# Performance work log

Measured on AMD Instinct MI355X. Metric: run time of the kernel, lower is better.

The kernel has to match this reference:

```python
import jax, jax.numpy as jnp
import numpy as np

LR = 0.1          # RMSprop learning rate (set_hyper_parameters)
ALPHA = 0.9       # RMSprop decay
ITERATIONS = 5    # SVGD iterations
INV_SIG2 = 1.0    # Gaussian posterior score scale (concrete post_grad)
EPS = 1e-8


def setup_inputs() -> dict:
    key = jax.random.key(0)
    k1, k2 = jax.random.split(key)
    x = jax.random.normal(k1, (8, 2048, 8), dtype=jnp.float32)          # [B, N, D] particles
    observation = jax.random.normal(k2, (8, 8), dtype=jnp.float32)      # [B, D]
    return {"x": x, "observation": observation}


def _svgd(x, observation):
    B, N, D = x.shape
    # median heuristic bandwidth h = median(pairwise dist)^2 / log(N), per batch, no-grad
    sq = jnp.sum((x[:, :, None, :] - x[:, None, :, :]) ** 2, axis=-1)   # [B, N, N]
    med = jnp.median(jnp.sqrt(sq).reshape(B, -1), axis=-1)              # [B]
    h = jax.lax.stop_gradient(med ** 2 / jnp.log(jnp.float32(N)))       # [B]
    inv_N = jnp.float32(1.0 / N)

    def post_grad(xc):
        # Gaussian posterior score: d/dx log N(x; observation, sigma^2 I)
        return (observation[:, None, :] - xc) * INV_SIG2                # [B, N, D]

    def step(carry, _):
        xc, s = carry
        dist = xc[:, :, None, :] - xc[:, None, :, :]                    # [B, i, j, D]
        K = jnp.exp(-jnp.sum(dist ** 2, axis=-1) / h[:, None, None])    # [B, i, j] rbf
        g = post_grad(xc)                                               # [B, j, D]
        # phi_i = (1/N) sum_j [ K_ij * g_j + (2/h)(x_i - x_j) K_ij ]
        phi = inv_N * (jnp.einsum('bij,bjd->bid', K, g)
                       + (2.0 / h)[:, None, None] * jnp.einsum('bij,bijd->bid', K, dist))
        # RMSprop (state update under no_grad in the original)
        s = jax.lax.stop_gradient(ALPHA * s + (1.0 - ALPHA) * phi ** 2)
        xc = xc + LR * phi / (jnp.sqrt(s) + EPS)
        return (xc, s), None

    (x, _), _ = jax.lax.scan(step, (x, jnp.zeros_like(x)), None, length=ITERATIONS)
    return x


def reference(x, observation):
    return _svgd(x, observation)
```

## Files before the change

### kernel.cpp

```cpp
#include <hip/hip_runtime.h>
#include <cstdint>

#define BATCH 8
#define NPART 2048
#define DDIM 8
#define NN (NPART * NPART)

#define MJCHUNK 128
#define SJCHUNK 512

constexpr float LR = 0.1f;
constexpr float ALPHA = 0.9f;
constexpr float EPS = 1e-8f;
constexpr float INV_N = 1.0f / (float)NPART;
constexpr float LOG2E = 1.44269504088896340736f;

typedef float v2f __attribute__((ext_vector_type(2)));
typedef float v4f __attribute__((ext_vector_type(4)));

__global__ __launch_bounds__(256) void init_ws_k(unsigned* __restrict__ hist,
                                                 unsigned* __restrict__ prefix,
                                                 unsigned* __restrict__ rank) {
    const int tid = blockIdx.x * 256 + threadIdx.x;
    if (tid < BATCH * 2 * 256) hist[tid] = 0u;
    if (tid < BATCH * 2) {
        prefix[tid] = 0u;
        rank[tid] = (unsigned)(NN / 2) + (unsigned)(tid & 1);
    }
}

__global__ __launch_bounds__(256) void median_hist_k(const float* __restrict__ x,
                                                     unsigned* __restrict__ hist,
                                                     const unsigned* __restrict__ prefix,
                                                     int shift) {
    __shared__ __align__(16) v4f xs0[MJCHUNK];
    __shared__ __align__(16) v4f xs1[MJCHUNK];
    __shared__ float rs[MJCHUNK];
    __shared__ unsigned lh[256 * 32];

    const int b = blockIdx.x;
    const int tid = threadIdx.x;
    const int lane = tid & 63;
    const int slot = tid & 31;
    const int trow = tid >> 6;
    const float* xb = x + (size_t)b * NPART * DDIM;

    const unsigned p0 = prefix[2 * b + 0];
    const unsigned p1 = prefix[2 * b + 1];
    const bool same = (p0 == p1);
    const unsigned mask = (shift == 24) ? 0u : (0xFFFFFFFFu << (shift + 8));

    const int nsel = same ? 1 : 2;
    for (int sel = 0; sel < nsel; ++sel) {
        const unsigned pref = sel ? p1 : p0;
        __syncthreads();
        for (int t = tid; t < 256 * 32; t += 256) lh[t] = 0u;

        for (int sp = 0; sp < 2; ++sp) {
            const int strip = sp ? (255 - (int)blockIdx.y) : (int)blockIdx.y;
            const int ibase = strip * 8 + trow * 2;
            v2f xi[2][4];
            float q[2];
#pragma unroll
            for (int rr = 0; rr < 2; ++rr) {
                const v4f t0 = ((const v4f*)(xb + (size_t)(ibase + rr) * DDIM))[0];
                const v4f t1 = ((const v4f*)(xb + (size_t)(ibase + rr) * DDIM))[1];
                xi[rr][0] = t0.xy; xi[rr][1] = t0.zw;
                xi[rr][2] = t1.xy; xi[rr][3] = t1.zw;
                q[rr] = t0.x * t0.x + t0.y * t0.y + t0.z * t0.z + t0.w * t0.w
                      + t1.x * t1.x + t1.y * t1.y + t1.z * t1.z + t1.w * t1.w;
            }
            const int c0 = (strip >> 4) * MJCHUNK;
            for (int cbase = c0; cbase < NPART; cbase += MJCHUNK) {
                __syncthreads();
                for (int t = tid; t < MJCHUNK; t += 256) {
                    const v4f u0 = ((const v4f*)(xb + (size_t)(cbase + t) * DDIM))[0];
                    const v4f u1 = ((const v4f*)(xb + (size_t)(cbase + t) * DDIM))[1];
                    xs0[t] = u0;
                    xs1[t] = u1;
                    rs[t] = u0.x * u0.x + u0.y * u0.y + u0.z * u0.z + u0.w * u0.w
                          + u1.x * u1.x + u1.y * u1.y + u1.z * u1.z + u1.w * u1.w;
                }
                __syncthreads();
#pragma unroll
                for (int j = lane; j < MJCHUNK; j += 64) {
                    const int jg = cbase + j;
                    const v4f A = xs0[j];
                    const v4f B = xs1[j];
                    const float r = rs[j];
                    const v2f A0 = A.xy, A1 = A.zw, B0 = B.xy, B1 = B.zw;
#pragma unroll
                    for (int rr = 0; rr < 2; ++rr) {
                        v2f p = A0 * xi[rr][0];
                        p += A1 * xi[rr][1];
                        p += B0 * xi[rr][2];
                        p += B1 * xi[rr][3];
                        const float sq = fmaxf(fmaf(-2.0f, p.x + p.y, q[rr] + r), 0.0f);
                        const unsigned u = __float_as_uint(sq);
                        if (jg > ibase + rr && (u & mask) == pref)
                            atomicAdd(&lh[((u >> shift) & 255u) * 32 + slot], 2u);
                    }
                }
            }
        }
        __syncthreads();
        unsigned tot = 0;
#pragma unroll
        for (int sct = 0; sct < 32; ++sct) tot += lh[tid * 32 + ((sct + tid) & 31)];
        if (tot) {
            atomicAdd(&hist[b * 512 + sel * 256 + tid], tot);
            if (same) atomicAdd(&hist[b * 512 + 256 + tid], tot);
        }
    }
}

__global__ void median_scan_k(unsigned* __restrict__ hist,
                              unsigned* __restrict__ prefix,
                              unsigned* __restrict__ rank,
                              int shift,
                              float* __restrict__ hpar) {
    __shared__ unsigned selv[16];
    const int t = threadIdx.x;
    if (t < 16) {
        const unsigned r = rank[t];
        const unsigned pref = prefix[t];
        const unsigned* hb = hist + t * 256;
        unsigned cum = 0;
        int bin = 0;
        for (; bin < 256; ++bin) {
            unsigned c = hb[bin];
            if (bin == 0 && pref == 0u) c += (unsigned)NPART;
            if (cum + c >= r) break;
            cum += c;
        }
        if (bin > 255) bin = 255;
        const unsigned np = pref | ((unsigned)bin << shift);
        prefix[t] = np;
        rank[t] = r - cum;
        selv[t] = np;
    }
    __syncthreads();
    for (int q = t; q < 16 * 256; q += 64) hist[q] = 0u;
    if (shift == 8 && t < BATCH) {
        const float v1 = __uint_as_float(selv[2 * t + 0]);
        const float v2 = __uint_as_float(selv[2 * t + 1]);
        const float med = 0.5f * (sqrtf(v1) + sqrtf(v2));
        const float h = (med * med) / logf((float)NPART);
        hpar[2 * t + 0] = -LOG2E / h;
        hpar[2 * t + 1] = 2.0f / h;
    }
}

__global__ __launch_bounds__(256, 4) void svgd_step_k(const float* __restrict__ x_in,
                                                      float* __restrict__ x_out,
                                                      float* __restrict__ s,
                                                      const float* __restrict__ hpar,
                                                      const float* __restrict__ obs,
                                                      int first) {
    __shared__ __align__(16) float smem[4608];
    v4f* xs0 = (v4f*)smem;
    v4f* xs1 = (v4f*)(smem + 2048);
    float* rs = smem + 4096;
    float (*part)[8][9] = (float (*)[8][9])smem;

    const int b = blockIdx.x;
    const int tid = threadIdx.x;
    const int lane = tid & 63;
    const int trow = tid >> 6;
    const float* xb = x_in + (size_t)b * NPART * DDIM;

    const float nih2 = hpar[2 * b + 0];
    const float c2 = hpar[2 * b + 1];
    const float cdot2 = -2.0f * nih2;

    const int ibase = blockIdx.y * 16 + trow * 4;
    v2f xi[4][4];
    float q[4];
#pragma unroll
    for (int rr = 0; rr < 4; ++rr) {
        const v4f t0 = ((const v4f*)(xb + (size_t)(ibase + rr) * DDIM))[0];
        const v4f t1 = ((const v4f*)(xb + (size_t)(ibase + rr) * DDIM))[1];
        xi[rr][0] = t0.xy; xi[rr][1] = t0.zw;
        xi[rr][2] = t1.xy; xi[rr][3] = t1.zw;
        q[rr] = nih2 * (t0.x * t0.x + t0.y * t0.y + t0.z * t0.z + t0.w * t0.w
                      + t1.x * t1.x + t1.y * t1.y + t1.z * t1.z + t1.w * t1.w);
    }

    float S0[4] = {0, 0, 0, 0};
    v2f V[4][4];
#pragma unroll
    for (int rr = 0; rr < 4; ++rr)
#pragma unroll
        for (int k = 0; k < 4; ++k) V[rr][k] = (v2f){0, 0};

    for (int cbase = 0; cbase < NPART; cbase += SJCHUNK) {
        __syncthreads();
        for (int t = tid; t < SJCHUNK; t += 256) {
            const v4f u0 = ((const v4f*)(xb + (size_t)(cbase + t) * DDIM))[0];
            const v4f u1 = ((const v4f*)(xb + (size_t)(cbase + t) * DDIM))[1];
            xs0[t] = u0;
            xs1[t] = u1;
            rs[t] = nih2 * (u0.x * u0.x + u0.y * u0.y + u0.z * u0.z + u0.w * u0.w
                          + u1.x * u1.x + u1.y * u1.y + u1.z * u1.z + u1.w * u1.w);
        }
        __syncthreads();
#pragma unroll 2
        for (int j = lane; j < SJCHUNK; j += 64) {
            const v4f A = xs0[j];
            const v4f B = xs1[j];
            const float r = rs[j];
            const v2f A0 = A.xy, A1 = A.zw, B0 = B.xy, B1 = B.zw;
#pragma unroll
            for (int rr = 0; rr < 4; ++rr) {
                v2f p = A0 * xi[rr][0];
                p += A1 * xi[rr][1];
                p += B0 * xi[rr][2];
                p += B1 * xi[rr][3];
                const float K = __builtin_amdgcn_exp2f(fmaf(cdot2, p.x + p.y, q[rr] + r));
                S0[rr] += K;
                const v2f K2 = {K, K};
                V[rr][0] += A0 * K2;
                V[rr][1] += A1 * K2;
                V[rr][2] += B0 * K2;
                V[rr][3] += B1 * K2;
            }
        }
    }

    __syncthreads();
#pragma unroll
    for (int rr = 0; rr < 4; ++rr) {
        float t0 = S0[rr];
        float t1 = V[rr][0].x, t2 = V[rr][0].y;
        float t3 = V[rr][1].x, t4 = V[rr][1].y;
        float t5 = V[rr][2].x, t6 = V[rr][2].y;
        float t7 = V[rr][3].x, t8 = V[rr][3].y;
        t0 += __shfl_xor(t0, 32); t0 += __shfl_xor(t0, 16); t0 += __shfl_xor(t0, 8);
        t1 += __shfl_xor(t1, 32); t1 += __shfl_xor(t1, 16); t1 += __shfl_xor(t1, 8);
        t2 += __shfl_xor(t2, 32); t2 += __shfl_xor(t2, 16); t2 += __shfl_xor(t2, 8);
        t3 += __shfl_xor(t3, 32); t3 += __shfl_xor(t3, 16); t3 += __shfl_xor(t3, 8);
        t4 += __shfl_xor(t4, 32); t4 += __shfl_xor(t4, 16); t4 += __shfl_xor(t4, 8);
        t5 += __shfl_xor(t5, 32); t5 += __shfl_xor(t5, 16); t5 += __shfl_xor(t5, 8);
        t6 += __shfl_xor(t6, 32); t6 += __shfl_xor(t6, 16); t6 += __shfl_xor(t6, 8);
        t7 += __shfl_xor(t7, 32); t7 += __shfl_xor(t7, 16); t7 += __shfl_xor(t7, 8);
        t8 += __shfl_xor(t8, 32); t8 += __shfl_xor(t8, 16); t8 += __shfl_xor(t8, 8);
        if (lane < 8) {
            const int row = trow * 4 + rr;
            part[row][lane][0] = t0;
            part[row][lane][1] = t1;
            part[row][lane][2] = t2;
            part[row][lane][3] = t3;
            part[row][lane][4] = t4;
            part[row][lane][5] = t5;
            part[row][lane][6] = t6;
            part[row][lane][7] = t7;
            part[row][lane][8] = t8;
        }
    }
    __syncthreads();

    if (tid < 128) {
        const int d2i = tid & 7;
        const int r2 = tid >> 3;
        const int i2 = blockIdx.y * 16 + r2;
        float S0t = 0.0f, Vt = 0.0f;
#pragma unroll
        for (int l = 0; l < 8; ++l) {
            S0t += part[r2][l][0];
            Vt += part[r2][l][1 + d2i];
        }
        const size_t idx = ((size_t)b * NPART + i2) * DDIM + d2i;
        const float xid = x_in[idx];
        const float obsd = obs[b * DDIM + d2i];
        const float U = fmaf(S0t, xid, -Vt);
        const float T = fmaf(S0t, obsd - xid, U);
        const float phi = INV_N * fmaf(c2, U, T);
        float sv;
        if (first) {
            sv = (1.0f - ALPHA) * phi * phi;
        } else {
            sv = ALPHA * s[idx] + (1.0f - ALPHA) * phi * phi;
        }
        s[idx] = sv;
        x_out[idx] = xid + LR * phi / (sqrtf(sv) + EPS);
    }
}

extern "C" void kernel_launch(void* const* d_in, const int* in_sizes, int n_in,
                              void* d_out, int out_size, void* d_ws, size_t ws_size,
                              hipStream_t stream) {
    const float* x0 = (const float*)d_in[0];
    const float* obs = (const float*)d_in[1];
    float* out = (float*)d_out;

    float* xa = (float*)d_ws;
    float* s = xa + BATCH * NPART * DDIM;
    unsigned* hist = (unsigned*)(s + BATCH * NPART * DDIM);
    unsigned* prefix = hist + BATCH * 2 * 256;
    unsigned* rank = prefix + BATCH * 2;
    float* hpar = (float*)(rank + BATCH * 2);

    init_ws_k<<<16, 256, 0, stream>>>(hist, prefix, rank);

    for (int r = 0; r < 3; ++r) {
        const int shift = 24 - 8 * r;
        median_hist_k<<<dim3(BATCH, 128), 256, 0, stream>>>(x0, hist, prefix, shift);
        median_scan_k<<<1, 64, 0, stream>>>(hist, prefix, rank, shift, hpar);
    }

    svgd_step_k<<<dim3(BATCH, 128), 256, 0, stream>>>(x0, out, s, hpar, obs, 1);
    svgd_step_k<<<dim3(BATCH, 128), 256, 0, stream>>>(out, xa, s, hpar, obs, 0);
    svgd_step_k<<<dim3(BATCH, 128), 256, 0, stream>>>(xa, out, s, hpar, obs, 0);
    svgd_step_k<<<dim3(BATCH, 128), 256, 0, stream>>>(out, xa, s, hpar, obs, 0);
    svgd_step_k<<<dim3(BATCH, 128), 256, 0, stream>>>(xa, out, s, hpar, obs, 0);
}
```

Baseline: 217.3 us.

## Compute pairwise RBF exponents with split-bf16 MFMA instead of scalar dot products

The SVGD step kernel now builds the exponent argument q_i + q_j - 2 x_i·x_j as a 32x32 matrix product on MFMA units. It splits each fp32 operand into bf16 high and low parts and uses three MFMAs to approximate fp32 accuracy. The norms are folded in through augmented columns. Each block now covers 32 rows with 512 threads, and each wave takes a 256-wide j range. The kernel reads x_j directly from global memory/L1 instead of staging it in LDS. This aims to offload the dot-product FLOPs from the VALU, at the risk of precision loss in the exponent and more uncoalesced global loads.

```diff
diff --git a/kernel.cpp b/kernel.cpp
--- a/kernel.cpp
+++ b/kernel.cpp
@@ -7,7 +7,6 @@
 #define NN (NPART * NPART)
 
 #define MJCHUNK 128
-#define SJCHUNK 512
 
 constexpr float LR = 0.1f;
 constexpr float ALPHA = 0.9f;
@@ -17,6 +16,17 @@
 
 typedef float v2f __attribute__((ext_vector_type(2)));
 typedef float v4f __attribute__((ext_vector_type(4)));
+typedef __attribute__((ext_vector_type(8))) short bf16x8;
+typedef __attribute__((ext_vector_type(16))) float f32x16;
+
+union FragU { bf16x8 v; unsigned u[4]; };
+
+__device__ __forceinline__ unsigned pk_bf16(float f0, float f1) {
+    return (__float_as_uint(f0) >> 16) | (__float_as_uint(f1) & 0xFFFF0000u);
+}
+__device__ __forceinline__ float btrunc(float f) {
+    return __uint_as_float(__float_as_uint(f) & 0xFFFF0000u);
+}
 
 __global__ __launch_bounds__(256) void init_ws_k(unsigned* __restrict__ hist,
                                                  unsigned* __restrict__ prefix,
@@ -151,123 +161,127 @@
     }
 }
 
-__global__ __launch_bounds__(256, 4) void svgd_step_k(const float* __restrict__ x_in,
+__global__ __launch_bounds__(512, 4) void svgd_step_k(const float* __restrict__ x_in,
                                                       float* __restrict__ x_out,
                                                       float* __restrict__ s,
                                                       const float* __restrict__ hpar,
                                                       const float* __restrict__ obs,
                                                       int first) {
-    __shared__ __align__(16) float smem[4608];
-    v4f* xs0 = (v4f*)smem;
-    v4f* xs1 = (v4f*)(smem + 2048);
-    float* rs = smem + 4096;
-    float (*part)[8][9] = (float (*)[8][9])smem;
+    __shared__ float part[32][16][9];
 
     const int b = blockIdx.x;
     const int tid = threadIdx.x;
-    const int lane = tid & 63;
-    const int trow = tid >> 6;
+    const int w = tid >> 6;
+    const int l = tid & 63;
+    const int col = l & 31;
+    const int half = l >> 5;
     const float* xb = x_in + (size_t)b * NPART * DDIM;
 
     const float nih2 = hpar[2 * b + 0];
     const float c2 = hpar[2 * b + 1];
-    const float cdot2 = -2.0f * nih2;
-
-    const int ibase = blockIdx.y * 16 + trow * 4;
-    v2f xi[4][4];
-    float q[4];
-#pragma unroll
-    for (int rr = 0; rr < 4; ++rr) {
-        const v4f t0 = ((const v4f*)(xb + (size_t)(ibase + rr) * DDIM))[0];
-        const v4f t1 = ((const v4f*)(xb + (size_t)(ibase + rr) * DDIM))[1];
-        xi[rr][0] = t0.xy; xi[rr][1] = t0.zw;
-        xi[rr][2] = t1.xy; xi[rr][3] = t1.zw;
-        q[rr] = nih2 * (t0.x * t0.x + t0.y * t0.y + t0.z * t0.z + t0.w * t0.w
-                      + t1.x * t1.x + t1.y * t1.y + t1.z * t1.z + t1.w * t1.w);
-    }
-
-    float S0[4] = {0, 0, 0, 0};
-    v2f V[4][4];
-#pragma unroll
-    for (int rr = 0; rr < 4; ++rr)
-#pragma unroll
-        for (int k = 0; k < 4; ++k) V[rr][k] = (v2f){0, 0};
-
-    for (int cbase = 0; cbase < NPART; cbase += SJCHUNK) {
-        __syncthreads();
-        for (int t = tid; t < SJCHUNK; t += 256) {
-            const v4f u0 = ((const v4f*)(xb + (size_t)(cbase + t) * DDIM))[0];
-            const v4f u1 = ((const v4f*)(xb + (size_t)(cbase + t) * DDIM))[1];
-            xs0[t] = u0;
-            xs1[t] = u1;
-            rs[t] = nih2 * (u0.x * u0.x + u0.y * u0.y + u0.z * u0.z + u0.w * u0.w
-                          + u1.x * u1.x + u1.y * u1.y + u1.z * u1.z + u1.w * u1.w);
-        }
-        __syncthreads();
-#pragma unroll 2
-        for (int j = lane; j < SJCHUNK; j += 64) {
-            const v4f A = xs0[j];
-            const v4f B = xs1[j];
-            const float r = rs[j];
-            const v2f A0 = A.xy, A1 = A.zw, B0 = B.xy, B1 = B.zw;
-#pragma unroll
-            for (int rr = 0; rr < 4; ++rr) {
-                v2f p = A0 * xi[rr][0];
-                p += A1 * xi[rr][1];
-                p += B0 * xi[rr][2];
-                p += B1 * xi[rr][3];
-                const float K = __builtin_amdgcn_exp2f(fmaf(cdot2, p.x + p.y, q[rr] + r));
-                S0[rr] += K;
-                const v2f K2 = {K, K};
-                V[rr][0] += A0 * K2;
-                V[rr][1] += A1 * K2;
-                V[rr][2] += B0 * K2;
-                V[rr][3] += B1 * K2;
+    const int ibase = blockIdx.y * 32;
+
+    FragU Bh, Bl;
+    {
+        const float* xi = xb + (size_t)(ibase + col) * DDIM;
+        const v4f t0 = ((const v4f*)xi)[0];
+        const v4f t1 = ((const v4f*)xi)[1];
+        const float qi = t0.x * t0.x + t0.y * t0.y + t0.z * t0.z + t0.w * t0.w
+                       + t1.x * t1.x + t1.y * t1.y + t1.z * t1.z + t1.w * t1.w;
+        if (half == 0) {
+            const float e0 = -2.0f * t0.x, e1 = -2.0f * t0.y;
+            const float e2 = -2.0f * t0.z, e3 = -2.0f * t0.w;
+            const float e4 = -2.0f * t1.x, e5 = -2.0f * t1.y;
+            const float e6 = -2.0f * t1.z, e7 = -2.0f * t1.w;
+            Bh.u[0] = pk_bf16(e0, e1);
+            Bh.u[1] = pk_bf16(e2, e3);
+            Bh.u[2] = pk_bf16(e4, e5);
+            Bh.u[3] = pk_bf16(e6, e7);
+            Bl.u[0] = pk_bf16(e0 - btrunc(e0), e1 - btrunc(e1));
+            Bl.u[1] = pk_bf16(e2 - btrunc(e2), e3 - btrunc(e3));
+            Bl.u[2] = pk_bf16(e4 - btrunc(e4), e5 - btrunc(e5));
+            Bl.u[3] = pk_bf16(e6 - btrunc(e6), e7 - btrunc(e7));
+        } else {
+            Bh.u[0] = pk_bf16(1.0f, qi);
+            Bl.u[0] = pk_bf16(0.0f, qi - btrunc(qi));
+            Bh.u[1] = Bh.u[2] = Bh.u[3] = 0u;
+            Bl.u[1] = Bl.u[2] = Bl.u[3] = 0u;
+        }
+    }
+
+    float S0 = 0.0f;
+    float V0 = 0, V1 = 0, V2 = 0, V3 = 0, V4 = 0, V5 = 0, V6 = 0, V7 = 0;
+
+    for (int t = 0; t < 8; ++t) {
+        const int jbase = w * 256 + t * 32;
+        FragU Ah, Al;
+        {
+            const float* xj = xb + (size_t)(jbase + col) * DDIM;
+            const v4f u0 = ((const v4f*)xj)[0];
+            const v4f u1 = ((const v4f*)xj)[1];
+            const float qj = u0.x * u0.x + u0.y * u0.y + u0.z * u0.z + u0.w * u0.w
+                           + u1.x * u1.x + u1.y * u1.y + u1.z * u1.z + u1.w * u1.w;
+            if (half == 0) {
+                Ah.u[0] = pk_bf16(u0.x, u0.y);
+                Ah.u[1] = pk_bf16(u0.z, u0.w);
+                Ah.u[2] = pk_bf16(u1.x, u1.y);
+                Ah.u[3] = pk_bf16(u1.z, u1.w);
+                Al.u[0] = pk_bf16(u0.x - btrunc(u0.x), u0.y - btrunc(u0.y));
+                Al.u[1] = pk_bf16(u0.z - btrunc(u0.z), u0.w - btrunc(u0.w));
+                Al.u[2] = pk_bf16(u1.x - btrunc(u1.x), u1.y - btrunc(u1.y));
+                Al.u[3] = pk_bf16(u1.z - btrunc(u1.z), u1.w - btrunc(u1.w));
+            } else {
+                Ah.u[0] = pk_bf16(qj, 1.0f);
+                Al.u[0] = pk_bf16(qj - btrunc(qj), 0.0f);
+                Ah.u[1] = Ah.u[2] = Ah.u[3] = 0u;
+                Al.u[1] = Al.u[2] = Al.u[3] = 0u;
             }
         }
-    }
-
+        f32x16 acc = {0, 0, 0, 0, 0, 0, 0, 0, 0, 0, 0, 0, 0, 0, 0, 0};
+        acc = __builtin_amdgcn_mfma_f32_32x32x16_bf16(Ah.v, Bh.v, acc, 0, 0, 0);
+        acc = __builtin_amdgcn_mfma_f32_32x32x16_bf16(Ah.v, Bl.v, acc, 0, 0, 0);
+        acc = __builtin_amdgcn_mfma_f32_32x32x16_bf16(Al.v, Bh.v, acc, 0, 0, 0);
+
+        const float* xrbase = xb + (size_t)(jbase + 4 * half) * DDIM;
+#pragma unroll
+        for (int reg = 0; reg < 16; ++reg) {
+            const int joff = (reg & 3) + 8 * (reg >> 2);
+            const float K = __builtin_amdgcn_exp2f(nih2 * acc[reg]);
+            const v4f a0 = ((const v4f*)(xrbase + (size_t)joff * DDIM))[0];
+            const v4f a1 = ((const v4f*)(xrbase + (size_t)joff * DDIM))[1];
+            S0 += K;
+            V0 = fmaf(K, a0.x, V0);
+            V1 = fmaf(K, a0.y, V1);
+            V2 = fmaf(K, a0.z, V2);
+            V3 = fmaf(K, a0.w, V3);
+            V4 = fmaf(K, a1.x, V4);
+            V5 = fmaf(K, a1.y, V5);
+            V6 = fmaf(K, a1.z, V6);
+            V7 = fmaf(K, a1.w, V7);
+        }
+    }
+
+    const int pslot = w * 2 + half;
+    part[col][pslot][0] = S0;
+    part[col][pslot][1] = V0;
+    part[col][pslot][2] = V1;
+    part[col][pslot][3] = V2;
+    part[col][pslot][4] = V3;
+    part[col][pslot][5] = V4;
+    part[col][pslot][6] = V5;
+    part[col][pslot][7] = V6;
+    part[col][pslot][8] = V7;
     __syncthreads();
-#pragma unroll
-    for (int rr = 0; rr < 4; ++rr) {
-        float t0 = S0[rr];
-        float t1 = V[rr][0].x, t2 = V[rr][0].y;
-        float t3 = V[rr][1].x, t4 = V[rr][1].y;
-        float t5 = V[rr][2].x, t6 = V[rr][2].y;
-        float t7 = V[rr][3].x, t8 = V[rr][3].y;
-        t0 += __shfl_xor(t0, 32); t0 += __shfl_xor(t0, 16); t0 += __shfl_xor(t0, 8);
-        t1 += __shfl_xor(t1, 32); t1 += __shfl_xor(t1, 16); t1 += __shfl_xor(t1, 8);
-        t2 += __shfl_xor(t2, 32); t2 += __shfl_xor(t2, 16); t2 += __shfl_xor(t2, 8);
-        t3 += __shfl_xor(t3, 32); t3 += __shfl_xor(t3, 16); t3 += __shfl_xor(t3, 8);
-        t4 += __shfl_xor(t4, 32); t4 += __shfl_xor(t4, 16); t4 += __shfl_xor(t4, 8);
-        t5 += __shfl_xor(t5, 32); t5 += __shfl_xor(t5, 16); t5 += __shfl_xor(t5, 8);
-        t6 += __shfl_xor(t6, 32); t6 += __shfl_xor(t6, 16); t6 += __shfl_xor(t6, 8);
-        t7 += __shfl_xor(t7, 32); t7 += __shfl_xor(t7, 16); t7 += __shfl_xor(t7, 8);
-        t8 += __shfl_xor(t8, 32); t8 += __shfl_xor(t8, 16); t8 += __shfl_xor(t8, 8);
-        if (lane < 8) {
-            const int row = trow * 4 + rr;
-            part[row][lane][0] = t0;
-            part[row][lane][1] = t1;
-            part[row][lane][2] = t2;
-            part[row][lane][3] = t3;
-            part[row][lane][4] = t4;
-            part[row][lane][5] = t5;
-            part[row][lane][6] = t6;
-            part[row][lane][7] = t7;
-            part[row][lane][8] = t8;
-        }
-    }
-    __syncthreads();
-
-    if (tid < 128) {
+
+    if (tid < 256) {
         const int d2i = tid & 7;
         const int r2 = tid >> 3;
-        const int i2 = blockIdx.y * 16 + r2;
+        const int i2 = ibase + r2;
         float S0t = 0.0f, Vt = 0.0f;
 #pragma unroll
-        for (int l = 0; l < 8; ++l) {
-            S0t += part[r2][l][0];
-            Vt += part[r2][l][1 + d2i];
+        for (int p = 0; p < 16; ++p) {
+            S0t += part[r2][p][0];
+            Vt += part[r2][p][1 + d2i];
         }
         const size_t idx = ((size_t)b * NPART + i2) * DDIM + d2i;
         const float xid = x_in[idx];
@@ -308,9 +322,9 @@
         median_scan_k<<<1, 64, 0, stream>>>(hist, prefix, rank, shift, hpar);
     }
 
-    svgd_step_k<<<dim3(BATCH, 128), 256, 0, stream>>>(x0, out, s, hpar, obs, 1);
-    svgd_step_k<<<dim3(BATCH, 128), 256, 0, stream>>>(out, xa, s, hpar, obs, 0);
-    svgd_step_k<<<dim3(BATCH, 128), 256, 0, stream>>>(xa, out, s, hpar, obs, 0);
-    svgd_step_k<<<dim3(BATCH, 128), 256, 0, stream>>>(out, xa, s, hpar, obs, 0);
-    svgd_step_k<<<dim3(BATCH, 128), 256, 0, stream>>>(xa, out, s, hpar, obs, 0);
-}
+    svgd_step_k<<<dim3(BATCH, 64), 512, 0, stream>>>(x0, out, s, hpar, obs, 1);
+    svgd_step_k<<<dim3(BATCH, 64), 512, 0, stream>>>(out, xa, s, hpar, obs, 0);
+    svgd_step_k<<<dim3(BATCH, 64), 512, 0, stream>>>(xa, out, s, hpar, obs, 0);
+    svgd_step_k<<<dim3(BATCH, 64), 512, 0, stream>>>(out, xa, s, hpar, obs, 0);
+    svgd_step_k<<<dim3(BATCH, 64), 512, 0, stream>>>(xa, out, s, hpar, obs, 0);
+}
```

Measured after the change: 273.4 us. 1.26x slower.

## Read particles directly from global memory and precompute scaled squared norms per step

Applied to the files above, without the earlier changes.

The inner j-loop now reads particle coordinates straight from global memory (cached in L1/L2) instead of staging 512-particle chunks into LDS with block barriers. The scaled squared norms per particle are computed once: first by a new small kernel for the initial positions, then in each step's epilogue through a shuffle reduction that writes them for the next step, ping-ponging between two buffers. This removes the per-block staging, redundant norm recomputation and __syncthreads. The cost is that every inner-loop load now hits the cache hierarchy rather than LDS.

```diff
diff --git a/kernel.cpp b/kernel.cpp
--- a/kernel.cpp
+++ b/kernel.cpp
@@ -7,7 +7,6 @@
 #define NN (NPART * NPART)
 
 #define MJCHUNK 128
-#define SJCHUNK 512
 
 constexpr float LR = 0.1f;
 constexpr float ALPHA = 0.9f;
@@ -151,23 +150,36 @@
     }
 }
 
+__global__ __launch_bounds__(256) void rs0_k(const float* __restrict__ x,
+                                             const float* __restrict__ hpar,
+                                             float* __restrict__ rs) {
+    const int row = blockIdx.x * 256 + threadIdx.x;
+    if (row < BATCH * NPART) {
+        const int b = row >> 11;
+        const float nih2 = hpar[2 * b + 0];
+        const v4f t0 = ((const v4f*)(x + (size_t)row * DDIM))[0];
+        const v4f t1 = ((const v4f*)(x + (size_t)row * DDIM))[1];
+        rs[row] = nih2 * (t0.x * t0.x + t0.y * t0.y + t0.z * t0.z + t0.w * t0.w
+                        + t1.x * t1.x + t1.y * t1.y + t1.z * t1.z + t1.w * t1.w);
+    }
+}
+
 __global__ __launch_bounds__(256, 4) void svgd_step_k(const float* __restrict__ x_in,
                                                       float* __restrict__ x_out,
                                                       float* __restrict__ s,
                                                       const float* __restrict__ hpar,
                                                       const float* __restrict__ obs,
+                                                      const float* __restrict__ rs_in,
+                                                      float* __restrict__ rs_out,
                                                       int first) {
-    __shared__ __align__(16) float smem[4608];
-    v4f* xs0 = (v4f*)smem;
-    v4f* xs1 = (v4f*)(smem + 2048);
-    float* rs = smem + 4096;
-    float (*part)[8][9] = (float (*)[8][9])smem;
+    __shared__ float part[16][8][9];
 
     const int b = blockIdx.x;
     const int tid = threadIdx.x;
     const int lane = tid & 63;
     const int trow = tid >> 6;
     const float* xb = x_in + (size_t)b * NPART * DDIM;
+    const float* rb = rs_in + (size_t)b * NPART;
 
     const float nih2 = hpar[2 * b + 0];
     const float c2 = hpar[2 * b + 1];
@@ -193,41 +205,28 @@
 #pragma unroll
         for (int k = 0; k < 4; ++k) V[rr][k] = (v2f){0, 0};
 
-    for (int cbase = 0; cbase < NPART; cbase += SJCHUNK) {
-        __syncthreads();
-        for (int t = tid; t < SJCHUNK; t += 256) {
-            const v4f u0 = ((const v4f*)(xb + (size_t)(cbase + t) * DDIM))[0];
-            const v4f u1 = ((const v4f*)(xb + (size_t)(cbase + t) * DDIM))[1];
-            xs0[t] = u0;
-            xs1[t] = u1;
-            rs[t] = nih2 * (u0.x * u0.x + u0.y * u0.y + u0.z * u0.z + u0.w * u0.w
-                          + u1.x * u1.x + u1.y * u1.y + u1.z * u1.z + u1.w * u1.w);
-        }
-        __syncthreads();
-#pragma unroll 2
-        for (int j = lane; j < SJCHUNK; j += 64) {
-            const v4f A = xs0[j];
-            const v4f B = xs1[j];
-            const float r = rs[j];
-            const v2f A0 = A.xy, A1 = A.zw, B0 = B.xy, B1 = B.zw;
-#pragma unroll
-            for (int rr = 0; rr < 4; ++rr) {
-                v2f p = A0 * xi[rr][0];
-                p += A1 * xi[rr][1];
-                p += B0 * xi[rr][2];
-                p += B1 * xi[rr][3];
-                const float K = __builtin_amdgcn_exp2f(fmaf(cdot2, p.x + p.y, q[rr] + r));
-                S0[rr] += K;
-                const v2f K2 = {K, K};
-                V[rr][0] += A0 * K2;
-                V[rr][1] += A1 * K2;
-                V[rr][2] += B0 * K2;
-                V[rr][3] += B1 * K2;
-            }
-        }
-    }
-
-    __syncthreads();
+#pragma unroll 4
+    for (int j = lane; j < NPART; j += 64) {
+        const v4f A = ((const v4f*)(xb + (size_t)j * DDIM))[0];
+        const v4f B = ((const v4f*)(xb + (size_t)j * DDIM))[1];
+        const float r = rb[j];
+        const v2f A0 = A.xy, A1 = A.zw, B0 = B.xy, B1 = B.zw;
+#pragma unroll
+        for (int rr = 0; rr < 4; ++rr) {
+            v2f p = A0 * xi[rr][0];
+            p += A1 * xi[rr][1];
+            p += B0 * xi[rr][2];
+            p += B1 * xi[rr][3];
+            const float K = __builtin_amdgcn_exp2f(fmaf(cdot2, p.x + p.y, q[rr] + r));
+            S0[rr] += K;
+            const v2f K2 = {K, K};
+            V[rr][0] += A0 * K2;
+            V[rr][1] += A1 * K2;
+            V[rr][2] += B0 * K2;
+            V[rr][3] += B1 * K2;
+        }
+    }
+
 #pragma unroll
     for (int rr = 0; rr < 4; ++rr) {
         float t0 = S0[rr];
@@ -282,7 +281,13 @@
             sv = ALPHA * s[idx] + (1.0f - ALPHA) * phi * phi;
         }
         s[idx] = sv;
-        x_out[idx] = xid + LR * phi / (sqrtf(sv) + EPS);
+        const float xn = xid + LR * phi / (sqrtf(sv) + EPS);
+        x_out[idx] = xn;
+        float sq = xn * xn;
+        sq += __shfl_xor(sq, 1);
+        sq += __shfl_xor(sq, 2);
+        sq += __shfl_xor(sq, 4);
+        if (d2i == 0) rs_out[(size_t)b * NPART + i2] = nih2 * sq;
     }
 }
 
@@ -299,6 +304,8 @@
     unsigned* prefix = hist + BATCH * 2 * 256;
     unsigned* rank = prefix + BATCH * 2;
     float* hpar = (float*)(rank + BATCH * 2);
+    float* rsA = hpar + BATCH * 2;
+    float* rsB = rsA + BATCH * NPART;
 
     init_ws_k<<<16, 256, 0, stream>>>(hist, prefix, rank);
 
@@ -308,9 +315,11 @@
         median_scan_k<<<1, 64, 0, stream>>>(hist, prefix, rank, shift, hpar);
     }
 
-    svgd_step_k<<<dim3(BATCH, 128), 256, 0, stream>>>(x0, out, s, hpar, obs, 1);
-    svgd_step_k<<<dim3(BATCH, 128), 256, 0, stream>>>(out, xa, s, hpar, obs, 0);
-    svgd_step_k<<<dim3(BATCH, 128), 256, 0, stream>>>(xa, out, s, hpar, obs, 0);
-    svgd_step_k<<<dim3(BATCH, 128), 256, 0, stream>>>(out, xa, s, hpar, obs, 0);
-    svgd_step_k<<<dim3(BATCH, 128), 256, 0, stream>>>(xa, out, s, hpar, obs, 0);
-}
+    rs0_k<<<64, 256, 0, stream>>>(x0, hpar, rsA);
+
+    svgd_step_k<<<dim3(BATCH, 128), 256, 0, stream>>>(x0, out, s, hpar, obs, rsA, rsB, 1);
+    svgd_step_k<<<dim3(BATCH, 128), 256, 0, stream>>>(out, xa, s, hpar, obs, rsB, rsA, 0);
+    svgd_step_k<<<dim3(BATCH, 128), 256, 0, stream>>>(xa, out, s, hpar, obs, rsA, rsB, 0);
+    svgd_step_k<<<dim3(BATCH, 128), 256, 0, stream>>>(out, xa, s, hpar, obs, rsB, rsA, 0);
+    svgd_step_k<<<dim3(BATCH, 128), 256, 0, stream>>>(xa, out, s, hpar, obs, rsA, rsB, 0);
+}
```

Result: no change. 215.1 us, median of 2 (-1.0%).
